# Optimization experiments

Hardware: AMD Instinct MI355X
Metric: run time of the kernel (lower is better)

Reference implementation:

```python
import jax, jax.numpy as jnp
import numpy as np

CLAMP = 1.0e4
MIN_DECAY = 0.001
MAX_DECAY = 0.999
EPS = 1e-06


def setup_inputs() -> dict:
    key = jax.random.key(0)
    ks = jax.random.split(key, 6)
    B, K, C = 8, 4096, 1024
    return {
        "tokens": jax.random.normal(ks[0], (B, K, C), dtype=jnp.float32),
        "state": jax.random.normal(ks[1], (B, C), dtype=jnp.float32),
        "decay_logit": jax.random.normal(ks[2], (C,), dtype=jnp.float32),
        "input_gain_raw": jax.random.normal(ks[3], (C,), dtype=jnp.float32),
        "output_gain_raw": jax.random.normal(ks[4], (C,), dtype=jnp.float32),
        "state_bias": jax.random.normal(ks[5], (C,), dtype=jnp.float32),
    }


def reference(tokens, state, decay_logit, input_gain_raw, output_gain_raw, state_bias):
    # constrained parameters, each [C]
    decay = MIN_DECAY + (MAX_DECAY - MIN_DECAY) * jax.nn.sigmoid(decay_logit)
    input_gain = jax.nn.softplus(input_gain_raw) + EPS
    output_gain = jax.nn.softplus(output_gain_raw) + EPS

    # sanitize inputs as in torch.nan_to_num(...).clamp(-1e4, 1e4)
    x = jnp.nan_to_num(tokens, nan=0.0, posinf=CLAMP, neginf=-CLAMP)
    x = jnp.clip(x, -CLAMP, CLAMP)

    one_minus_decay = 1.0 - decay
    # driven_t = input_gain * x_t + state_bias, computed for all steps at once: [B,K,C]
    driven = input_gain[None, None, :] * x + state_bias[None, None, :]
    b = one_minus_decay[None, None, :] * driven  # additive term per step

    def step(s, b_t):  # s: [B,C], b_t: [B,C]
        s_new = decay[None, :] * s + b_t
        return s_new, s_new

    # scan over time axis K
    final_state, states = jax.lax.scan(step, state, jnp.swapaxes(b, 0, 1))
    outputs = output_gain[None, None, :] * jnp.swapaxes(states, 0, 1)  # [B,K,C]
    return outputs, final_state
```

## Files before the change

### kernel.cpp

```cpp
#include <hip/hip_runtime.h>
#include <math.h>

namespace {

constexpr int kB = 8;
constexpr int kK = 4096;
constexpr int kC = 1024;
constexpr int kL = 64;
constexpr int kNC = kK / kL;
constexpr int kNBLK = kB * kNC;
constexpr int kTPB = 256;

constexpr float kClamp = 1.0e4f;
constexpr float kMinD = 0.001f;
constexpr float kMaxD = 0.999f;
constexpr float kEps = 1e-6f;

typedef float f4 __attribute__((ext_vector_type(4)));

__device__ __forceinline__ float sanitize(float x) {
  x = (x != x) ? 0.0f : x;
  return fminf(kClamp, fmaxf(-kClamp, x));
}

__device__ __forceinline__ float softplusf(float x) {
  return fmaxf(x, 0.0f) + log1pf(expf(-fabsf(x)));
}

__device__ __forceinline__ float decay_of(float logit) {
  return kMinD + (kMaxD - kMinD) / (1.0f + expf(-logit));
}

union f2u {
  unsigned long long u;
  float f[2];
};

__global__ void k_init(int* __restrict__ flags) {
  const int i = blockIdx.x * blockDim.x + threadIdx.x;
  if (i < kNBLK) flags[i] = 0;
}

__global__ __launch_bounds__(kTPB) void k_scan(
    const float* __restrict__ tokens, const float* __restrict__ state,
    const float* __restrict__ dlog, const float* __restrict__ igr,
    const float* __restrict__ ogr, const float* __restrict__ sbias,
    float* __restrict__ out, float* __restrict__ final_out,
    unsigned long long* __restrict__ carry, int* __restrict__ flags) {
  const int gid = blockIdx.x;
  const int b = gid / kNC;
  const int j = gid - b * kNC;
  const int c0 = threadIdx.x * 4;

  const f4 dl = *reinterpret_cast<const f4*>(dlog + c0);
  const f4 ig = *reinterpret_cast<const f4*>(igr + c0);
  const f4 og = *reinterpret_cast<const f4*>(ogr + c0);
  const f4 sb = *reinterpret_cast<const f4*>(sbias + c0);

  const float d0 = decay_of(dl.x), d1 = decay_of(dl.y);
  const float d2 = decay_of(dl.z), d3 = decay_of(dl.w);
  const float g0 = softplusf(ig.x) + kEps, g1 = softplusf(ig.y) + kEps;
  const float g2 = softplusf(ig.z) + kEps, g3 = softplusf(ig.w) + kEps;
  const float a0 = (1.0f - d0) * g0, a1 = (1.0f - d1) * g1;
  const float a2 = (1.0f - d2) * g2, a3 = (1.0f - d3) * g3;
  const float bb0 = (1.0f - d0) * sb.x, bb1 = (1.0f - d1) * sb.y;
  const float bb2 = (1.0f - d2) * sb.z, bb3 = (1.0f - d3) * sb.w;
  const float o0 = softplusf(og.x) + kEps, o1 = softplusf(og.y) + kEps;
  const float o2 = softplusf(og.z) + kEps, o3 = softplusf(og.w) + kEps;

  const float* tp = tokens + (((size_t)b * kK) + (size_t)j * kL) * kC + c0;

  float s0 = 0.0f, s1 = 0.0f, s2 = 0.0f, s3 = 0.0f;
  for (int i = 0; i < kL; i += 8) {
    f4 x[8];
#pragma unroll
    for (int u = 0; u < 8; ++u)
      x[u] = *reinterpret_cast<const f4*>(tp + (size_t)(i + u) * kC);
#pragma unroll
    for (int u = 0; u < 8; ++u) {
      s0 = fmaf(d0, s0, fmaf(a0, sanitize(x[u].x), bb0));
      s1 = fmaf(d1, s1, fmaf(a1, sanitize(x[u].y), bb1));
      s2 = fmaf(d2, s2, fmaf(a2, sanitize(x[u].z), bb2));
      s3 = fmaf(d3, s3, fmaf(a3, sanitize(x[u].w), bb3));
    }
  }
  {
    const size_t ci = ((size_t)gid * kC + c0) / 2;
    f2u lo, hi;
    lo.f[0] = s0; lo.f[1] = s1; hi.f[0] = s2; hi.f[1] = s3;
    __hip_atomic_store(carry + ci, lo.u, __ATOMIC_RELAXED,
                       __HIP_MEMORY_SCOPE_AGENT);
    __hip_atomic_store(carry + ci + 1, hi.u, __ATOMIC_RELAXED,
                       __HIP_MEMORY_SCOPE_AGENT);
  }
  __syncthreads();
  if (threadIdx.x == 0) {
    __hip_atomic_store(flags + gid, 1, __ATOMIC_RELAXED,
                       __HIP_MEMORY_SCOPE_AGENT);
  }

  const int base = b * kNC;
  if (threadIdx.x < j) {
    while (__hip_atomic_load(flags + base + threadIdx.x, __ATOMIC_RELAXED,
                             __HIP_MEMORY_SCOPE_AGENT) == 0) {
      __builtin_amdgcn_s_sleep(2);
    }
  }
  __syncthreads();

  float dL0 = d0, dL1 = d1, dL2 = d2, dL3 = d3;
#pragma unroll
  for (int i = 0; i < 6; ++i) {
    dL0 *= dL0; dL1 *= dL1; dL2 *= dL2; dL3 *= dL3;
  }

  const f4 st = *reinterpret_cast<const f4*>(state + (size_t)b * kC + c0);
  float S0 = st.x, S1 = st.y, S2 = st.z, S3 = st.w;
#pragma unroll 8
  for (int p = 0; p < j; ++p) {
    const size_t ci = ((size_t)(base + p) * kC + c0) / 2;
    f2u lo, hi;
    lo.u = __hip_atomic_load(carry + ci, __ATOMIC_RELAXED,
                             __HIP_MEMORY_SCOPE_AGENT);
    hi.u = __hip_atomic_load(carry + ci + 1, __ATOMIC_RELAXED,
                             __HIP_MEMORY_SCOPE_AGENT);
    S0 = fmaf(dL0, S0, lo.f[0]);
    S1 = fmaf(dL1, S1, lo.f[1]);
    S2 = fmaf(dL2, S2, hi.f[0]);
    S3 = fmaf(dL3, S3, hi.f[1]);
  }

  float* op = out + (((size_t)b * kK) + (size_t)j * kL) * kC + c0;
  s0 = S0; s1 = S1; s2 = S2; s3 = S3;
  for (int i = 0; i < kL; i += 8) {
    f4 x[8];
#pragma unroll
    for (int u = 0; u < 8; ++u)
      x[u] = *reinterpret_cast<const f4*>(tp + (size_t)(i + u) * kC);
#pragma unroll
    for (int u = 0; u < 8; ++u) {
      s0 = fmaf(d0, s0, fmaf(a0, sanitize(x[u].x), bb0));
      s1 = fmaf(d1, s1, fmaf(a1, sanitize(x[u].y), bb1));
      s2 = fmaf(d2, s2, fmaf(a2, sanitize(x[u].z), bb2));
      s3 = fmaf(d3, s3, fmaf(a3, sanitize(x[u].w), bb3));
      f4 y; y.x = o0 * s0; y.y = o1 * s1; y.z = o2 * s2; y.w = o3 * s3;
      *reinterpret_cast<f4*>(op + (size_t)(i + u) * kC) = y;
    }
  }

  if (j == kNC - 1) {
    f4 fv; fv.x = s0; fv.y = s1; fv.z = s2; fv.w = s3;
    *reinterpret_cast<f4*>(final_out + (size_t)b * kC + c0) = fv;
  }
}

}

extern "C" void kernel_launch(void* const* d_in, const int* in_sizes, int n_in,
                              void* d_out, int out_size, void* d_ws, size_t ws_size,
                              hipStream_t stream) {
  const float* tokens = (const float*)d_in[0];
  const float* state  = (const float*)d_in[1];
  const float* dlog   = (const float*)d_in[2];
  const float* igr    = (const float*)d_in[3];
  const float* ogr    = (const float*)d_in[4];
  const float* sbias  = (const float*)d_in[5];

  float* out = (float*)d_out;
  float* final_out = out + (size_t)kB * kK * kC;

  unsigned long long* carry = (unsigned long long*)d_ws;
  int* flags = (int*)((char*)d_ws + (size_t)kNBLK * kC * sizeof(float));

  k_init<<<dim3((kNBLK + 255) / 256), 256, 0, stream>>>(flags);
  k_scan<<<dim3(kNBLK), kTPB, 0, stream>>>(tokens, state, dlog, igr, ogr,
                                           sbias, out, final_out, carry, flags);
}
```

Measured before the change: 76.76 us.

## Keep local scan states in fp16 registers instead of re-reading tokens

The first pass now stores each step's local partial state as packed fp16 in registers. After the carry-in is resolved, outputs are rebuilt as o*local + o*d^t*S_in, so the second read of the token chunk from memory is gone. Threads now cover 2 channels each with 512 threads per block, and an acquire fence is added after the flag wait. The fp16 storage of the partial states lowers accuracy, and the 64-entry register array raises register pressure.

After: 87.69 us. 14.2% more time.

```diff
diff --git a/kernel.cpp b/kernel.cpp
--- a/kernel.cpp
+++ b/kernel.cpp
@@ -9,14 +9,15 @@
 constexpr int kL = 64;
 constexpr int kNC = kK / kL;
 constexpr int kNBLK = kB * kNC;
-constexpr int kTPB = 256;
+constexpr int kTPB = 512;
 
 constexpr float kClamp = 1.0e4f;
 constexpr float kMinD = 0.001f;
 constexpr float kMaxD = 0.999f;
 constexpr float kEps = 1e-6f;
 
-typedef float f4 __attribute__((ext_vector_type(4)));
+typedef float f2 __attribute__((ext_vector_type(2)));
+typedef _Float16 h2 __attribute__((ext_vector_type(2)));
 
 __device__ __forceinline__ float sanitize(float x) {
   x = (x != x) ? 0.0f : x;
@@ -50,48 +51,43 @@
   const int gid = blockIdx.x;
   const int b = gid / kNC;
   const int j = gid - b * kNC;
-  const int c0 = threadIdx.x * 4;
+  const int c0 = threadIdx.x * 2;
 
-  const f4 dl = *reinterpret_cast<const f4*>(dlog + c0);
-  const f4 ig = *reinterpret_cast<const f4*>(igr + c0);
-  const f4 og = *reinterpret_cast<const f4*>(ogr + c0);
-  const f4 sb = *reinterpret_cast<const f4*>(sbias + c0);
+  const f2 dl = *reinterpret_cast<const f2*>(dlog + c0);
+  const f2 ig = *reinterpret_cast<const f2*>(igr + c0);
+  const f2 og = *reinterpret_cast<const f2*>(ogr + c0);
+  const f2 sb = *reinterpret_cast<const f2*>(sbias + c0);
 
   const float d0 = decay_of(dl.x), d1 = decay_of(dl.y);
-  const float d2 = decay_of(dl.z), d3 = decay_of(dl.w);
   const float g0 = softplusf(ig.x) + kEps, g1 = softplusf(ig.y) + kEps;
-  const float g2 = softplusf(ig.z) + kEps, g3 = softplusf(ig.w) + kEps;
   const float a0 = (1.0f - d0) * g0, a1 = (1.0f - d1) * g1;
-  const float a2 = (1.0f - d2) * g2, a3 = (1.0f - d3) * g3;
   const float bb0 = (1.0f - d0) * sb.x, bb1 = (1.0f - d1) * sb.y;
-  const float bb2 = (1.0f - d2) * sb.z, bb3 = (1.0f - d3) * sb.w;
   const float o0 = softplusf(og.x) + kEps, o1 = softplusf(og.y) + kEps;
-  const float o2 = softplusf(og.z) + kEps, o3 = softplusf(og.w) + kEps;
 
   const float* tp = tokens + (((size_t)b * kK) + (size_t)j * kL) * kC + c0;
 
-  float s0 = 0.0f, s1 = 0.0f, s2 = 0.0f, s3 = 0.0f;
-  for (int i = 0; i < kL; i += 8) {
-    f4 x[8];
+  h2 loc[kL];
+  float s0 = 0.0f, s1 = 0.0f;
+#pragma unroll
+  for (int i0 = 0; i0 < kL; i0 += 8) {
+    f2 x[8];
 #pragma unroll
     for (int u = 0; u < 8; ++u)
-      x[u] = *reinterpret_cast<const f4*>(tp + (size_t)(i + u) * kC);
+      x[u] = *reinterpret_cast<const f2*>(tp + (size_t)(i0 + u) * kC);
 #pragma unroll
     for (int u = 0; u < 8; ++u) {
       s0 = fmaf(d0, s0, fmaf(a0, sanitize(x[u].x), bb0));
       s1 = fmaf(d1, s1, fmaf(a1, sanitize(x[u].y), bb1));
-      s2 = fmaf(d2, s2, fmaf(a2, sanitize(x[u].z), bb2));
-      s3 = fmaf(d3, s3, fmaf(a3, sanitize(x[u].w), bb3));
+      h2 h; h.x = (_Float16)s0; h.y = (_Float16)s1;
+      loc[i0 + u] = h;
     }
   }
+  const float cv0 = s0, cv1 = s1;
+
   {
-    const size_t ci = ((size_t)gid * kC + c0) / 2;
-    f2u lo, hi;
-    lo.f[0] = s0; lo.f[1] = s1; hi.f[0] = s2; hi.f[1] = s3;
-    __hip_atomic_store(carry + ci, lo.u, __ATOMIC_RELAXED,
-                       __HIP_MEMORY_SCOPE_AGENT);
-    __hip_atomic_store(carry + ci + 1, hi.u, __ATOMIC_RELAXED,
-                       __HIP_MEMORY_SCOPE_AGENT);
+    f2u cu; cu.f[0] = cv0; cu.f[1] = cv1;
+    __hip_atomic_store(carry + ((size_t)gid * kC + c0) / 2, cu.u,
+                       __ATOMIC_RELAXED, __HIP_MEMORY_SCOPE_AGENT);
   }
   __syncthreads();
   if (threadIdx.x == 0) {
@@ -107,50 +103,40 @@
     }
   }
   __syncthreads();
+  __builtin_amdgcn_fence(__ATOMIC_ACQUIRE, "agent");
 
-  float dL0 = d0, dL1 = d1, dL2 = d2, dL3 = d3;
+  float dL0 = d0, dL1 = d1;
 #pragma unroll
-  for (int i = 0; i < 6; ++i) {
-    dL0 *= dL0; dL1 *= dL1; dL2 *= dL2; dL3 *= dL3;
-  }
+  for (int i = 0; i < 6; ++i) { dL0 *= dL0; dL1 *= dL1; }
 
-  const f4 st = *reinterpret_cast<const f4*>(state + (size_t)b * kC + c0);
-  float S0 = st.x, S1 = st.y, S2 = st.z, S3 = st.w;
+  const f2 st = *reinterpret_cast<const f2*>(state + (size_t)b * kC + c0);
+  float S0 = st.x, S1 = st.y;
 #pragma unroll 8
   for (int p = 0; p < j; ++p) {
-    const size_t ci = ((size_t)(base + p) * kC + c0) / 2;
-    f2u lo, hi;
-    lo.u = __hip_atomic_load(carry + ci, __ATOMIC_RELAXED,
-                             __HIP_MEMORY_SCOPE_AGENT);
-    hi.u = __hip_atomic_load(carry + ci + 1, __ATOMIC_RELAXED,
-                             __HIP_MEMORY_SCOPE_AGENT);
-    S0 = fmaf(dL0, S0, lo.f[0]);
-    S1 = fmaf(dL1, S1, lo.f[1]);
-    S2 = fmaf(dL2, S2, hi.f[0]);
-    S3 = fmaf(dL3, S3, hi.f[1]);
+    f2u cu;
+    cu.u = __hip_atomic_load(carry + ((size_t)(base + p) * kC + c0) / 2,
+                             __ATOMIC_RELAXED, __HIP_MEMORY_SCOPE_AGENT);
+    S0 = fmaf(dL0, S0, cu.f[0]);
+    S1 = fmaf(dL1, S1, cu.f[1]);
   }
 
   float* op = out + (((size_t)b * kK) + (size_t)j * kL) * kC + c0;
-  s0 = S0; s1 = S1; s2 = S2; s3 = S3;
-  for (int i = 0; i < kL; i += 8) {
-    f4 x[8];
+  float P0 = o0 * S0, P1 = o1 * S1;
 #pragma unroll
-    for (int u = 0; u < 8; ++u)
-      x[u] = *reinterpret_cast<const f4*>(tp + (size_t)(i + u) * kC);
-#pragma unroll
-    for (int u = 0; u < 8; ++u) {
-      s0 = fmaf(d0, s0, fmaf(a0, sanitize(x[u].x), bb0));
-      s1 = fmaf(d1, s1, fmaf(a1, sanitize(x[u].y), bb1));
-      s2 = fmaf(d2, s2, fmaf(a2, sanitize(x[u].z), bb2));
-      s3 = fmaf(d3, s3, fmaf(a3, sanitize(x[u].w), bb3));
-      f4 y; y.x = o0 * s0; y.y = o1 * s1; y.z = o2 * s2; y.w = o3 * s3;
-      *reinterpret_cast<f4*>(op + (size_t)(i + u) * kC) = y;
-    }
+  for (int i = 0; i < kL; ++i) {
+    P0 *= d0; P1 *= d1;
+    const h2 h = loc[i];
+    f2 y;
+    y.x = fmaf(o0, (float)h.x, P0);
+    y.y = fmaf(o1, (float)h.y, P1);
+    *reinterpret_cast<f2*>(op + (size_t)i * kC) = y;
   }
 
   if (j == kNC - 1) {
-    f4 fv; fv.x = s0; fv.y = s1; fv.z = s2; fv.w = s3;
-    *reinterpret_cast<f4*>(final_out + (size_t)b * kC + c0) = fv;
+    f2 fv;
+    fv.x = fmaf(dL0, S0, cv0);
+    fv.y = fmaf(dL1, S1, cv1);
+    *reinterpret_cast<f2*>(final_out + (size_t)b * kC + c0) = fv;
   }
 }
 
```
